# Kernel optimization log

Hardware: AMD Instinct MI355X
Metric: run time of the kernel (lower is better)

The kernel has to match this reference:

```python
import jax, jax.numpy as jnp
import numpy as np

BATCHING_INFO = {0: {'max_tokens': 16, 'batching_range': (0, 16)},
                 1: {'max_tokens': 32, 'batching_range': (16, 32)},
                 2: {'max_tokens': 48, 'batching_range': (32, 100000)}}
WINDOW_SHAPE = (10, 10, 4)
SPARSE_SHAPE = (400, 400, 16)
POS_TEMPERATURE = 1000.0
N_VOXELS = 300000
FEAT_DIM = 192


def get_window_coors_np(coors, sparse_shape, window_shape, do_shift):
    wx, wy, wz = window_shape
    sx, sy, sz = sparse_shape
    mx = int(np.ceil(sx / wx) + 1)
    my = int(np.ceil(sy / wy) + 1)
    mz = int(np.ceil(sz / wz) + 1)
    mper = mx * my * mz
    if do_shift:
        shx, shy, shz = wx // 2, wy // 2, wz // 2
    else:
        shx, shy, shz = wx, wy, wz
    if wz == sz:
        shz = 0
    scx = coors[:, 3] + shx
    scy = coors[:, 2] + shy
    scz = coors[:, 1] + shz
    wcx = scx // wx
    wcy = scy // wy
    wcz = scz // wz
    batch_win_inds = coors[:, 0] * mper + wcx * my * mz + wcy * mz + wcz
    coors_in_win = np.stack([scz % wz, scy % wy, scx % wx], axis=-1)
    return batch_win_inds, coors_in_win


def get_inner_win_inds_np(win_inds):
    # rank of each voxel within its window, stable w.r.t. original order
    n = len(win_inds)
    order = np.argsort(win_inds, kind='stable')
    sw = win_inds[order]
    starts = np.r_[0, np.flatnonzero(np.diff(sw)) + 1]
    counts = np.diff(np.r_[starts, n])
    ranks = np.arange(n) - np.repeat(starts, counts)
    inner = np.empty(n, dtype=np.int64)
    inner[order] = ranks
    return inner


def batching_single_shift(batch_win_inds):
    lvl = -np.ones_like(batch_win_inds)
    inner = get_inner_win_inds_np(batch_win_inds)
    bincount = np.bincount(batch_win_inds)
    num_before = bincount[batch_win_inds]
    target = np.zeros_like(batch_win_inds)
    for bl, info in BATCHING_INFO.items():
        lo, hi = info['batching_range']
        m = (num_before >= lo) & (num_before < hi)
        target[m] = info['max_tokens']
        lvl[m] = bl
    return inner < target, lvl


def get_flat2win_inds_np(batch_win_inds, lvl):
    d = {}
    for dl, info in BATCHING_INFO.items():
        m = lvl == dl
        if not m.any():
            continue
        sub = batch_win_inds[m]
        uniq, conti = np.unique(sub, return_inverse=True)
        inner = get_inner_win_inds_np(sub)
        d[dl] = (conti * info['max_tokens'] + inner, np.flatnonzero(m), len(uniq))
    d['voxel_batching_level'] = lvl
    return d


def partition_indices(coors):
    # full window partition + two-shift voxel batching (pure int logic)
    bwi0, ciw0 = get_window_coors_np(coors, SPARSE_SHAPE, WINDOW_SHAPE, False)
    bwi1, ciw1 = get_window_coors_np(coors, SPARSE_SHAPE, WINDOW_SHAPE, True)
    keep0, lvl0 = batching_single_shift(bwi0)
    idx = np.flatnonzero(keep0)
    lvl0 = lvl0[keep0]
    bwi0 = bwi0[keep0]
    bwi1k = bwi1[keep0]
    keep1, lvl1 = batching_single_shift(bwi1k)
    idx = idx[keep1]
    lvl0 = lvl0[keep1]
    bwi0 = bwi0[keep1]
    lvl1 = lvl1[keep1]
    bwi1k = bwi1k[keep1]
    inds0 = get_flat2win_inds_np(bwi0, lvl0)
    inds1 = get_flat2win_inds_np(bwi1k, lvl1)
    return idx, ciw0[idx], ciw1[idx], inds0, inds1


def get_pos_embed(coors_in_win, feat_dim):
    wx, wy, wz = WINDOW_SHAPE
    c = jnp.asarray(coors_in_win, jnp.float32)
    z = c[:, 0] - wz / 2.0
    y = c[:, 1] - wy / 2.0
    x = c[:, 2] - wx / 2.0
    pos_length = feat_dim // 3
    i = jnp.arange(pos_length, dtype=jnp.float32)
    inv_freq = jnp.power(jnp.float32(POS_TEMPERATURE), 2.0 * jnp.floor(i / 2.0) / pos_length)

    def emb(v):
        e = v[:, None] / inv_freq[None, :]
        return jnp.stack([jnp.sin(e[:, ::2]), jnp.cos(e[:, 1::2])], axis=-1).reshape(e.shape[0], -1)

    return jnp.concatenate([emb(x), emb(y), emb(z)], axis=-1)


def flat2window(feat, inds_dict):
    out = {}
    for dl in sorted(k for k in inds_dict if isinstance(k, int)):
        flat_inds, pos, nwin = inds_dict[dl]
        T = BATCHING_INFO[dl]['max_tokens']
        buf = jnp.zeros((nwin * T, feat.shape[-1]), feat.dtype)
        buf = buf.at[jnp.asarray(flat_inds)].set(feat[jnp.asarray(pos)])
        out[dl] = buf.reshape(nwin, T, feat.shape[-1])
    return out


def setup_inputs() -> dict:
    key = jax.random.key(0)
    rng = np.random.default_rng(0)
    b = rng.integers(0, 2, N_VOXELS)
    z = rng.integers(0, SPARSE_SHAPE[2], N_VOXELS)
    y = rng.integers(0, SPARSE_SHAPE[1], N_VOXELS)
    x = rng.integers(0, SPARSE_SHAPE[0], N_VOXELS)
    coords = np.stack([b, z, y, x], axis=1).astype(np.int64)
    feats = jax.random.normal(key, (N_VOXELS, FEAT_DIM), jnp.float32)
    return {'voxel_features': feats, 'voxel_coords': jnp.asarray(coords)}


def reference(voxel_features, voxel_coords):
    coors = np.asarray(voxel_coords)
    idx, ciw0, ciw1, inds0, inds1 = partition_indices(coors)
    idx_j = jnp.asarray(idx)
    feats = voxel_features[idx_j]
    coords_kept = jnp.asarray(coors[idx])
    outs = [feats, coords_kept]
    for ciw, inds in ((ciw0, inds0), (ciw1, inds1)):
        pe = get_pos_embed(ciw, voxel_features.shape[1])
        pe_dict = flat2window(pe, inds)
        for dl in sorted(k for k in inds if isinstance(k, int)):
            outs.append(pe_dict[dl])
        for dl in sorted(k for k in inds if isinstance(k, int)):
            flat_inds, pos, nwin = inds[dl]
            T = BATCHING_INFO[dl]['max_tokens']
            filled = jnp.zeros((nwin * T,), bool).at[jnp.asarray(flat_inds)].set(True)
            outs.append(jnp.logical_not(filled).reshape(nwin, T))  # key_padding_mask
    return tuple(outs)
```

## Files before the change

kernel.cpp:

```cpp
#include <hip/hip_runtime.h>
#include <math.h>

typedef unsigned int u32;
typedef unsigned short u16;
typedef __attribute__((ext_vector_type(4))) float f32x4;

#define WTOT 16810
#define MPER 8405
#define MAXROWS (WTOT * 48)

#define M_NKEPT 0
#define M_NWIN0 1
#define M_NWIN1 4
#define M_WORDS 16

__device__ __forceinline__ int level_of(int c) {
    if (c < 16) return 0;
    if (c < 32) return 1;
    return 2;
}
__device__ __forceinline__ int target_of(int lvl) {
    return (lvl == 0) ? 16 : ((lvl == 1) ? 32 : 48);
}

__device__ __forceinline__ int wave_incl_scan(int v) {
#pragma unroll
    for (int o = 1; o < 64; o <<= 1) {
        int t = __shfl_up(v, o, 64);
        if ((int)(threadIdx.x & 63) >= o) v += t;
    }
    return v;
}

__device__ __forceinline__ int block_incl_scan_1024(int v, int* wsums, int* total) {
    int lane = threadIdx.x & 63, wid = threadIdx.x >> 6;
    int iv = wave_incl_scan(v);
    if (lane == 63) wsums[wid] = iv;
    __syncthreads();
    if (wid == 0) {
        int s = (lane < 16) ? wsums[lane] : 0;
        s = wave_incl_scan(s);
        if (lane < 16) wsums[lane] = s;
    }
    __syncthreads();
    int add = (wid > 0) ? wsums[wid - 1] : 0;
    int incl = iv + add;
    *total = wsums[15];
    __syncthreads();
    return incl;
}

__device__ __forceinline__ int block_is64(const int* c32, int* sh) {
    if (threadIdx.x < 64) {
        unsigned long long b = __ballot(c32[2 * threadIdx.x + 1] != 0);
        if (threadIdx.x == 0) *sh = (b == 0ULL) ? 1 : 0;
    }
    __syncthreads();
    return *sh;
}

__device__ __forceinline__ int list_rank(const u32* list, int lcount, u32 key, int t) {
    int local = 0;
    int L4 = (lcount + 3) >> 2;
    const uint4* l4 = (const uint4*)list;
    for (int p = 0; p < L4; p++) {
        uint4 e = l4[p];
        local += ((e.x & ~1023u) == key && (int)(e.x & 1023u) < t);
        local += ((e.y & ~1023u) == key && (int)(e.y & 1023u) < t);
        local += ((e.z & ~1023u) == key && (int)(e.z & 1023u) < t);
        local += ((e.w & ~1023u) == key && (int)(e.w & 1023u) < t);
    }
    return local;
}


__global__ __launch_bounds__(256) void k_wincoords(const void* coors_raw, int N, int NB,
        int CE2, int* bwi0, int* bwi1, int* ciw0, int* ciw1, u32* H0, float* dict) {
    __shared__ int s64;
    if ((int)blockIdx.x >= NB) {
        int e = ((int)blockIdx.x - NB) * 256 + (int)threadIdx.x;
        if (e < 76800) {
            int idx = e / 192;
            int j = e - idx * 192;
            int dz = idx & 3;
            int dy = (idx >> 2) % 10;
            int dx = (idx >> 2) / 10;
            int sel = j >> 6;
            float v = (sel == 0) ? ((float)dx - 5.0f)
                    : ((sel == 1) ? ((float)dy - 5.0f) : ((float)dz - 2.0f));
            int kk = (j & 63) >> 1;
            float invf = (float)exp(6.907755278982137 * (double)kk / 32.0);
            float a = v / invf;
            dict[e] = (j & 1) ? cosf(a) : sinf(a);
        }
        return;
    }
    int is64 = block_is64((const int*)coors_raw, &s64);
    int i = (int)blockIdx.x * 256 + (int)threadIdx.x;
    if (i >= N) return;
    int b, z, y, x;
    if (is64) {
        const long long* c = (const long long*)coors_raw;
        long long o = 4LL * i;
        b = (int)c[o]; z = (int)c[o + 1]; y = (int)c[o + 2]; x = (int)c[o + 3];
    } else {
        const int* c = (const int*)coors_raw;
        b = c[4 * i]; z = c[4 * i + 1]; y = c[4 * i + 2]; x = c[4 * i + 3];
    }
    int ch = i >> 10;
    {
        int scx = x + 10, scy = y + 10, scz = z + 4;
        int w = b * MPER + (scx / 10) * 205 + (scy / 10) * 5 + (scz >> 2);
        bwi0[i] = w;
        ciw0[i] = (scz & 3) | ((scy % 10) << 8) | ((scx % 10) << 16);
        atomicAdd(&H0[(size_t)w * CE2 + (ch >> 1)], 1u << ((ch & 1) * 16));
    }
    {
        int scx = x + 5, scy = y + 5, scz = z + 2;
        int w = b * MPER + (scx / 10) * 205 + (scy / 10) * 5 + (scz >> 2);
        bwi1[i] = w;
        ciw1[i] = (scz & 3) | ((scy % 10) << 8) | ((scx % 10) << 16);
    }
}

__global__ __launch_bounds__(256) void k_prefix16(u32* H, u16* counts, int CE2, int NW) {
    int w = ((int)blockIdx.x * 256 + (int)threadIdx.x) >> 6;
    int lane = threadIdx.x & 63;
    if (w >= NW) return;
    u32* row = H + (size_t)w * CE2;
    u32 run = 0;
    for (int p0 = 0; p0 < CE2; p0 += 64) {
        int p = p0 + lane;
        u32 v = (p < CE2) ? row[p] : 0u;
        u32 lo = v & 0xffffu, hi = v >> 16;
        int s = (int)(lo + hi);
        int incl = wave_incl_scan(s);
        u32 excl = (u32)(incl - s);
        u32 offlo = run + excl;
        u32 offhi = offlo + lo;
        if (offlo > 1023u) offlo = 1023u;
        if (offhi > 1023u) offhi = 1023u;
        if (p < CE2) row[p] = offlo | (offhi << 16);
        int tot = __shfl(incl, 63, 64);
        run += (u32)tot;
        if (run > 1023u) run = 1023u;
    }
    if (lane == 0) counts[w] = (u16)run;
}

__global__ __launch_bounds__(1024) void k_stage1(const int* bwi0, const int* bwi1,
        const u16* counts0, const u16* H0_16, u32* H1, int* keep0, int N, int CE, int CE2) {
    __shared__ alignas(16) u32 list[1028];
    __shared__ int lcount;
    int c = blockIdx.x, t = threadIdx.x;
    int i = (c << 10) + t;
    if (t == 0) lcount = 0;
    __syncthreads();
    int w0 = -1, cur = 0, cnt = 0;
    if (i < N) {
        w0 = bwi0[i];
        size_t ro = (size_t)w0 * CE + c;
        cur = (int)H0_16[ro];
        int nxt = (c + 1 < CE) ? (int)H0_16[ro + 1] : (int)counts0[w0];
        cnt = nxt - cur;
        if (cnt >= 2) { int p = atomicAdd(&lcount, 1); list[p] = ((u32)w0 << 10) | (u32)t; }
    }
    __syncthreads();
    if (t < 3) list[lcount + t] = 0xFFFFFFFFu;
    __syncthreads();
    if (i >= N) return;
    int local = (cnt >= 2) ? list_rank(list, lcount, (u32)w0 << 10, t) : 0;
    int k0 = (cur + local) < target_of(level_of((int)counts0[w0]));
    keep0[i] = k0;
    if (k0) atomicAdd(&H1[(size_t)bwi1[i] * CE2 + (c >> 1)], 1u << ((c & 1) * 16));
}

__global__ __launch_bounds__(1024) void k_stage2(const int* bwi0, const int* bwi1,
        const int* keep0, const u16* counts1k, const u16* H1_16,
        u32* HF0, u32* HF1, int* keepf, int* chunkcnt, int N, int CE, int CE2) {
    __shared__ alignas(16) u32 list[1028];
    __shared__ int lcount, blksum;
    int c = blockIdx.x, t = threadIdx.x;
    int i = (c << 10) + t;
    int k0 = (i < N) ? keep0[i] : 0;
    if (t == 0) { lcount = 0; blksum = 0; }
    __syncthreads();
    int w1 = -1, cur = 0, cnt = 0;
    if (k0) {
        w1 = bwi1[i];
        size_t ro = (size_t)w1 * CE + c;
        cur = (int)H1_16[ro];
        int nxt = (c + 1 < CE) ? (int)H1_16[ro + 1] : (int)counts1k[w1];
        cnt = nxt - cur;
        if (cnt >= 2) { int p = atomicAdd(&lcount, 1); list[p] = ((u32)w1 << 10) | (u32)t; }
    }
    __syncthreads();
    if (t < 3) list[lcount + t] = 0xFFFFFFFFu;
    __syncthreads();
    int kf = 0;
    if (k0) {
        int local = (cnt >= 2) ? list_rank(list, lcount, (u32)w1 << 10, t) : 0;
        kf = (cur + local) < target_of(level_of((int)counts1k[w1]));
    }
    if (i < N) keepf[i] = kf;
    if (kf) {
        atomicAdd(&HF0[(size_t)bwi0[i] * CE2 + (c >> 1)], 1u << ((c & 1) * 16));
        atomicAdd(&HF1[(size_t)w1 * CE2 + (c >> 1)], 1u << ((c & 1) * 16));
    }
    unsigned long long b = __ballot(kf);
    if ((t & 63) == 0) atomicAdd(&blksum, __popcll(b));
    __syncthreads();
    if (t == 0) chunkcnt[c] = blksum;
}

__global__ __launch_bounds__(1024) void k_midscan(int* chunkcnt, int C, int* meta,
        const u16* counts0, const u16* fcount0, int* conti0,
        const u16* counts1, const u16* fcount1, int* conti1) {
    __shared__ int wsums[16];
    __shared__ int running;
    __shared__ int run3[3];
    if (blockIdx.x == 0) {
        if (threadIdx.x == 0) running = 0;
        __syncthreads();
        for (int base = 0; base < C; base += 1024) {
            int i = base + threadIdx.x;
            int v = (i < C) ? chunkcnt[i] : 0;
            int total;
            int incl = block_incl_scan_1024(v, wsums, &total);
            int run = running;
            if (i < C) chunkcnt[i] = run + incl - v;
            __syncthreads();
            if (threadIdx.x == 0) running = run + total;
            __syncthreads();
        }
        if (threadIdx.x == 0) meta[M_NKEPT] = running;
    } else {
        const u16* counts = (blockIdx.x == 2) ? counts1 : counts0;
        const u16* fcount = (blockIdx.x == 2) ? fcount1 : fcount0;
        int* conti = (blockIdx.x == 2) ? conti1 : conti0;
        int* nwin_out = meta + ((blockIdx.x == 2) ? M_NWIN1 : M_NWIN0);
        if (threadIdx.x < 3) run3[threadIdx.x] = 0;
        __syncthreads();
        for (int base = 0; base < WTOT; base += 1024) {
            int i = base + threadIdx.x;
            int c = (i < WTOT) ? (int)counts[i] : 0;
            int f = (i < WTOT) ? (int)fcount[i] : 0;
            int lvl = level_of(c);
            int act = (c > 0 && f > 0) ? 1 : 0;
            int packed = act ? (1 << (11 * lvl)) : 0;
            int total;
            int incl = block_incl_scan_1024(packed, wsums, &total);
            int excl = incl - packed;
            int r0 = run3[0], r1 = run3[1], r2 = run3[2];
            if (i < WTOT) {
                int e;
                if (lvl == 0) e = r0 + (excl & 2047);
                else if (lvl == 1) e = r1 + ((excl >> 11) & 2047);
                else e = r2 + ((excl >> 22) & 2047);
                conti[i] = e;
            }
            __syncthreads();
            if (threadIdx.x == 0) {
                run3[0] = r0 + (total & 2047);
                run3[1] = r1 + ((total >> 11) & 2047);
                run3[2] = r2 + ((total >> 22) & 2047);
            }
            __syncthreads();
        }
        if (threadIdx.x < 3) nwin_out[threadIdx.x] = run3[threadIdx.x];
    }
}

__global__ __launch_bounds__(1024) void k_stage3(const int* bwi0, const int* bwi1,
        const int* ciw0, const int* ciw1, const int* keepf,
        const u16* counts0, const u16* counts1k,
        const int* conti0, const int* conti1,
        const u16* HF0_16, const u16* HF1_16,
        const u16* fcount0, const u16* fcount1,
        const int* chunkpref, const int* meta,
        int* idxarr, int* rowvox0, int* rowvox1, int N, int CE) {
    __shared__ alignas(16) u32 list0[1028];
    __shared__ alignas(16) u32 list1[1028];
    __shared__ int lc0, lc1, wsum[16];
    int c = blockIdx.x, t = threadIdx.x, lane = t & 63, wv = t >> 6;
    int i = (c << 10) + t;
    if (t == 0) { lc0 = 0; lc1 = 0; }
    int kf = (i < N) ? keepf[i] : 0;
    unsigned long long m = __ballot(kf);
    if (lane == 0) wsum[wv] = __popcll(m);
    __syncthreads();
    if (t < 64) {
        int s = (t < 16) ? wsum[t] : 0;
        s = wave_incl_scan(s);
        if (t < 16) wsum[t] = s;
    }
    __syncthreads();
    int lk = (wv ? wsum[wv - 1] : 0) + __popcll(m & ((1ull << lane) - 1ull));
    int w0 = -1, w1 = -1, cur0 = 0, cur1 = 0, cnt0 = 0, cnt1 = 0;
    if (kf) {
        w0 = bwi0[i]; w1 = bwi1[i];
        size_t r0o = (size_t)w0 * CE + c;
        cur0 = (int)HF0_16[r0o];
        int nxt0 = (c + 1 < CE) ? (int)HF0_16[r0o + 1] : (int)fcount0[w0];
        cnt0 = nxt0 - cur0;
        if (cnt0 >= 2) { int p = atomicAdd(&lc0, 1); list0[p] = ((u32)w0 << 10) | (u32)t; }
        size_t r1o = (size_t)w1 * CE + c;
        cur1 = (int)HF1_16[r1o];
        int nxt1 = (c + 1 < CE) ? (int)HF1_16[r1o + 1] : (int)fcount1[w1];
        cnt1 = nxt1 - cur1;
        if (cnt1 >= 2) { int p = atomicAdd(&lc1, 1); list1[p] = ((u32)w1 << 10) | (u32)t; }
    }
    __syncthreads();
    if (t < 3) { list0[lc0 + t] = 0xFFFFFFFFu; list1[lc1 + t] = 0xFFFFFFFFu; }
    __syncthreads();
    if (!kf) return;
    int l0 = (cnt0 >= 2) ? list_rank(list0, lc0, (u32)w0 << 10, t) : 0;
    int l1 = (cnt1 >= 2) ? list_rank(list1, lc1, (u32)w1 << 10, t) : 0;
    int innerF0 = cur0 + l0;
    int innerF1 = cur1 + l1;
    idxarr[chunkpref[c] + lk] = i;
    int n00 = meta[M_NWIN0], n01 = meta[M_NWIN0 + 1];
    int n10 = meta[M_NWIN1], n11 = meta[M_NWIN1 + 1];
    {
        int lvl = level_of((int)counts0[w0]);
        int T = target_of(lvl);
        int rb = (lvl == 0) ? 0 : ((lvl == 1) ? n00 * 16 : (n00 * 16 + n01 * 32));
        rowvox0[rb + conti0[w0] * T + innerF0] = ciw0[i];
    }
    {
        int lvl = level_of((int)counts1k[w1]);
        int T = target_of(lvl);
        int rb = (lvl == 0) ? 0 : ((lvl == 1) ? n10 * 16 : (n10 * 16 + n11 * 32));
        rowvox1[rb + conti1[w1] * T + innerF1] = ciw1[i];
    }
}

__global__ __launch_bounds__(256) void k_render(const float* feats, const void* coors_raw,
        const int* meta, const int* idxarr, const int* rowvox0, const int* rowvox1,
        const float* dict, float* out, int NA) {
    __shared__ int s64;
    int nk = meta[M_NKEPT];
    int n00 = meta[M_NWIN0], n01 = meta[M_NWIN0 + 1], n02 = meta[M_NWIN0 + 2];
    int n10 = meta[M_NWIN1], n11 = meta[M_NWIN1 + 1], n12 = meta[M_NWIN1 + 2];
    int R0 = n00 * 16 + n01 * 32 + n02 * 48;
    int R1 = n10 * 16 + n11 * 32 + n12 * 48;
    int obuf0 = nk * 196;
    int omask0 = obuf0 + R0 * 192;
    int obuf1 = omask0 + R0;
    int omask1 = obuf1 + R1 * 192;
    int ototal = omask1 + R1;
    if ((int)blockIdx.x < NA) {
        int is64 = block_is64((const int*)coors_raw, &s64);
        int ocoor = nk * 192;
        const f32x4* src = (const f32x4*)feats;
        f32x4* dst = (f32x4*)out;
        int tot = nk * 52;
        int step = NA * 256;
        for (int idx = (int)blockIdx.x * 256 + (int)threadIdx.x; idx < tot; idx += step) {
            if (idx < nk * 48) {
                int row = idx / 48;
                int col = idx - row * 48;
                f32x4 v = src[(size_t)idxarr[row] * 48 + col];
                __builtin_nontemporal_store(v, dst + idx);
            } else {
                int cidx = idx - nk * 48;
                int k = cidx >> 2, tt = cidx & 3;
                int ii = idxarr[k];
                int v = is64 ? (int)((const long long*)coors_raw)[4LL * ii + tt]
                             : ((const int*)coors_raw)[4 * ii + tt];
                out[ocoor + cidx] = (float)v;
            }
        }
    } else {
        int q0 = obuf0 >> 2, q1 = ototal >> 2;
        const f32x4* dict4 = (const f32x4*)dict;
        f32x4* out4 = (f32x4*)out;
        int step = ((int)gridDim.x - NA) * 256;
        for (int q = q0 + ((int)blockIdx.x - NA) * 256 + (int)threadIdx.x; q < q1; q += step) {
            int e = q << 2;
            f32x4 val;
            bool pe1 = (e >= obuf1) && (e < omask1);
            if ((e < omask0) || pe1) {
                unsigned rel = (unsigned)(e - (pe1 ? obuf1 : obuf0));
                unsigned row = rel / 192u;
                unsigned j = rel - row * 192u;
                int ciw = pe1 ? rowvox1[row] : rowvox0[row];
                if (ciw < 0) {
                    val = (f32x4){0.0f, 0.0f, 0.0f, 0.0f};
                } else {
                    int di = (ciw & 3) + ((ciw >> 8) & 15) * 4 + ((ciw >> 16) & 15) * 40;
                    val = dict4[di * 48 + (int)(j >> 2)];
                }
            } else {
                int base = (e >= omask1) ? omask1 : omask0;
                const int* rv = (e >= omask1) ? rowvox1 : rowvox0;
                int4 c4 = *(const int4*)(rv + (e - base));
                val.x = (c4.x < 0) ? 1.0f : 0.0f;
                val.y = (c4.y < 0) ? 1.0f : 0.0f;
                val.z = (c4.z < 0) ? 1.0f : 0.0f;
                val.w = (c4.w < 0) ? 1.0f : 0.0f;
            }
            __builtin_nontemporal_store(val, out4 + q);
        }
    }
}

extern "C" void kernel_launch(void* const* d_in, const int* in_sizes, int n_in,
                              void* d_out, int out_size, void* d_ws, size_t ws_size,
                              hipStream_t stream) {
    const float* feats = (const float*)d_in[0];
    const void* coors = d_in[1];
    int N = in_sizes[0] / 192;
    int C = (N + 1023) >> 10;
    int CE = (C + 1) & ~1;
    int CE2 = CE >> 1;
    size_t TW32 = (size_t)WTOT * CE2;
    int N4 = (N + 3) & ~3;

    u32* U = (u32*)d_ws;
    int* bwi0 = (int*)U;            int* bwi1 = bwi0 + N4;
    int* ciw0 = bwi1 + N4;          int* ciw1 = ciw0 + N4;
    int* keep0 = ciw1 + N4;         int* keepf = keep0 + N4;
    int* idxarr = keepf + N4;
    u32* H0 = (u32*)(idxarr + N4);
    u32* H1 = H0 + TW32;
    u32* HF0 = H1 + TW32;
    u32* HF1 = HF0 + TW32;
    u16* counts0 = (u16*)(HF1 + TW32);
    u16* counts1k = (u16*)((u32*)counts0 + 8408);
    u16* fcount0 = (u16*)((u32*)counts1k + 8408);
    u16* fcount1 = fcount0 + WTOT;
    int* chunkcnt = (int*)((u32*)fcount0 + 16812);
    int CP4 = (C + 3) & ~3;
    int* conti0 = chunkcnt + CP4;
    int* conti1 = conti0 + 16812;
    int* rowvox0 = conti1 + 16812;
    int* rowvox1 = rowvox0 + MAXROWS;
    int* meta = rowvox1 + MAXROWS;
    float* dict = (float*)(meta + M_WORDS);

    int nb256 = (N + 255) / 256;

    hipMemsetAsync(H0, 0, 4 * TW32 * sizeof(u32), stream);
    hipMemsetAsync(rowvox0, 0xFF, (size_t)2 * MAXROWS * sizeof(int), stream);

    k_wincoords<<<nb256 + 300, 256, 0, stream>>>(coors, N, nb256, CE2,
                                                 bwi0, bwi1, ciw0, ciw1, H0, dict);

    int pgrid = (WTOT * 64 + 255) / 256;
    k_prefix16<<<pgrid, 256, 0, stream>>>(H0, counts0, CE2, WTOT);
    k_stage1<<<C, 1024, 0, stream>>>(bwi0, bwi1, counts0, (const u16*)H0, H1, keep0, N, CE, CE2);

    k_prefix16<<<pgrid, 256, 0, stream>>>(H1, counts1k, CE2, WTOT);
    k_stage2<<<C, 1024, 0, stream>>>(bwi0, bwi1, keep0, counts1k, (const u16*)H1,
                                     HF0, HF1, keepf, chunkcnt, N, CE, CE2);

    k_prefix16<<<2 * pgrid, 256, 0, stream>>>(HF0, fcount0, CE2, 2 * WTOT);
    k_midscan<<<3, 1024, 0, stream>>>(chunkcnt, C, meta,
                                      counts0, fcount0, conti0,
                                      counts1k, fcount1, conti1);

    k_stage3<<<C, 1024, 0, stream>>>(bwi0, bwi1, ciw0, ciw1, keepf, counts0, counts1k,
                                     conti0, conti1, (const u16*)HF0, (const u16*)HF1,
                                     fcount0, fcount1, chunkcnt, meta,
                                     idxarr, rowvox0, rowvox1, N, CE);

    k_render<<<4096, 256, 0, stream>>>(feats, coors, meta, idxarr, rowvox0, rowvox1,
                                       dict, (float*)d_out, 1536);

    (void)n_in; (void)ws_size; (void)out_size;
}
```

Measured before the change: 1.193 ms.

## Pack per-window chunk histograms into 8-bit counters and keep-flags into ballot bitmasks

Per-window/per-chunk histograms now use four 8-bit counters per word instead of two 16-bit ones, halving histogram memory and the memset. Keep flags are stored as per-wave 64-bit ballot masks instead of int arrays. The rowvox 0xFF fill is folded into a prefix-scan launch, replacing a separate memset. Coordinate loads are vectorised and the feature gather uses non-temporal loads. 8-bit prefix offsets saturate at 255, which risks wrong ranks if a window holds more than 255 voxels before a chunk.

```diff
diff --git a/kernel.cpp b/kernel.cpp
--- a/kernel.cpp
+++ b/kernel.cpp
@@ -3,7 +3,10 @@
 
 typedef unsigned int u32;
 typedef unsigned short u16;
+typedef unsigned char u8;
+typedef unsigned long long u64;
 typedef __attribute__((ext_vector_type(4))) float f32x4;
+typedef __attribute__((ext_vector_type(4))) int i32x4;
 
 #define WTOT 16810
 #define MPER 8405
@@ -75,7 +78,7 @@
 
 
 __global__ __launch_bounds__(256) void k_wincoords(const void* coors_raw, int N, int NB,
-        int CE2, int* bwi0, int* bwi1, int* ciw0, int* ciw1, u32* H0, float* dict) {
+        int CE4, int* bwi0, int* bwi1, int* ciw0, int* ciw1, u32* H0, float* dict) {
     __shared__ int s64;
     if ((int)blockIdx.x >= NB) {
         int e = ((int)blockIdx.x - NB) * 256 + (int)threadIdx.x;
@@ -99,13 +102,14 @@
     int i = (int)blockIdx.x * 256 + (int)threadIdx.x;
     if (i >= N) return;
     int b, z, y, x;
+    const i32x4* c4 = (const i32x4*)coors_raw;
     if (is64) {
-        const long long* c = (const long long*)coors_raw;
-        long long o = 4LL * i;
-        b = (int)c[o]; z = (int)c[o + 1]; y = (int)c[o + 2]; x = (int)c[o + 3];
+        i32x4 q0 = c4[2 * (size_t)i];
+        i32x4 q1 = c4[2 * (size_t)i + 1];
+        b = q0.x; z = q0.z; y = q1.x; x = q1.z;
     } else {
-        const int* c = (const int*)coors_raw;
-        b = c[4 * i]; z = c[4 * i + 1]; y = c[4 * i + 2]; x = c[4 * i + 3];
+        i32x4 q = c4[i];
+        b = q.x; z = q.y; y = q.z; x = q.w;
     }
     int ch = i >> 10;
     {
@@ -113,7 +117,7 @@
         int w = b * MPER + (scx / 10) * 205 + (scy / 10) * 5 + (scz >> 2);
         bwi0[i] = w;
         ciw0[i] = (scz & 3) | ((scy % 10) << 8) | ((scx % 10) << 16);
-        atomicAdd(&H0[(size_t)w * CE2 + (ch >> 1)], 1u << ((ch & 1) * 16));
+        atomicAdd(&H0[(size_t)w * CE4 + (ch >> 2)], 1u << ((ch & 3) * 8));
     }
     {
         int scx = x + 5, scy = y + 5, scz = z + 2;
@@ -123,74 +127,87 @@
     }
 }
 
-__global__ __launch_bounds__(256) void k_prefix16(u32* H, u16* counts, int CE2, int NW) {
+__global__ __launch_bounds__(256) void k_prefix8(u32* H, u16* counts, int CE4, int NW,
+                                                 int PB, int* fillPtr, int fillN4) {
+    if ((int)blockIdx.x >= PB) {
+        int idx = ((int)blockIdx.x - PB) * 256 + (int)threadIdx.x;
+        if (idx < fillN4) {
+            i32x4 v = (i32x4){-1, -1, -1, -1};
+            __builtin_nontemporal_store(v, ((i32x4*)fillPtr) + idx);
+        }
+        return;
+    }
     int w = ((int)blockIdx.x * 256 + (int)threadIdx.x) >> 6;
     int lane = threadIdx.x & 63;
     if (w >= NW) return;
-    u32* row = H + (size_t)w * CE2;
-    u32 run = 0;
-    for (int p0 = 0; p0 < CE2; p0 += 64) {
+    u32* row = H + (size_t)w * CE4;
+    int run = 0;
+    for (int p0 = 0; p0 < CE4; p0 += 64) {
         int p = p0 + lane;
-        u32 v = (p < CE2) ? row[p] : 0u;
-        u32 lo = v & 0xffffu, hi = v >> 16;
-        int s = (int)(lo + hi);
+        u32 v = (p < CE4) ? row[p] : 0u;
+        int b0 = (int)(v & 255u), b1 = (int)((v >> 8) & 255u);
+        int b2 = (int)((v >> 16) & 255u), b3 = (int)(v >> 24);
+        int s = b0 + b1 + b2 + b3;
         int incl = wave_incl_scan(s);
-        u32 excl = (u32)(incl - s);
-        u32 offlo = run + excl;
-        u32 offhi = offlo + lo;
-        if (offlo > 1023u) offlo = 1023u;
-        if (offhi > 1023u) offhi = 1023u;
-        if (p < CE2) row[p] = offlo | (offhi << 16);
-        int tot = __shfl(incl, 63, 64);
-        run += (u32)tot;
-        if (run > 1023u) run = 1023u;
+        int base = run + incl - s;
+        int e0 = base, e1 = base + b0, e2 = e1 + b1, e3 = e2 + b2;
+        u32 o0 = (u32)(e0 > 255 ? 255 : e0);
+        u32 o1 = (u32)(e1 > 255 ? 255 : e1);
+        u32 o2 = (u32)(e2 > 255 ? 255 : e2);
+        u32 o3 = (u32)(e3 > 255 ? 255 : e3);
+        if (p < CE4) row[p] = o0 | (o1 << 8) | (o2 << 16) | (o3 << 24);
+        run += __shfl(incl, 63, 64);
+        if (run > 1023) run = 1023;
     }
     if (lane == 0) counts[w] = (u16)run;
 }
 
 __global__ __launch_bounds__(1024) void k_stage1(const int* bwi0, const int* bwi1,
-        const u16* counts0, const u16* H0_16, u32* H1, int* keep0, int N, int CE, int CE2) {
+        const u16* counts0, const u8* H0b, u32* H1, u64* km0, int N, int CB, int CE4) {
     __shared__ alignas(16) u32 list[1028];
     __shared__ int lcount;
-    int c = blockIdx.x, t = threadIdx.x;
+    int c = blockIdx.x, t = threadIdx.x, lane = t & 63, wv = t >> 6;
     int i = (c << 10) + t;
     if (t == 0) lcount = 0;
     __syncthreads();
     int w0 = -1, cur = 0, cnt = 0;
     if (i < N) {
         w0 = bwi0[i];
-        size_t ro = (size_t)w0 * CE + c;
-        cur = (int)H0_16[ro];
-        int nxt = (c + 1 < CE) ? (int)H0_16[ro + 1] : (int)counts0[w0];
+        size_t ro = (size_t)w0 * CB + c;
+        cur = (int)H0b[ro];
+        int nxt = (c + 1 < CB) ? (int)H0b[ro + 1] : (int)counts0[w0];
         cnt = nxt - cur;
         if (cnt >= 2) { int p = atomicAdd(&lcount, 1); list[p] = ((u32)w0 << 10) | (u32)t; }
     }
     __syncthreads();
     if (t < 3) list[lcount + t] = 0xFFFFFFFFu;
     __syncthreads();
-    if (i >= N) return;
-    int local = (cnt >= 2) ? list_rank(list, lcount, (u32)w0 << 10, t) : 0;
-    int k0 = (cur + local) < target_of(level_of((int)counts0[w0]));
-    keep0[i] = k0;
-    if (k0) atomicAdd(&H1[(size_t)bwi1[i] * CE2 + (c >> 1)], 1u << ((c & 1) * 16));
+    int k0 = 0;
+    if (i < N) {
+        int local = (cnt >= 2) ? list_rank(list, lcount, (u32)w0 << 10, t) : 0;
+        k0 = (cur + local) < target_of(level_of((int)counts0[w0]));
+    }
+    u64 bal = __ballot(k0);
+    if (lane == 0) km0[((size_t)c << 4) + wv] = bal;
+    if (k0) atomicAdd(&H1[(size_t)bwi1[i] * CE4 + (c >> 2)], 1u << ((c & 3) * 8));
 }
 
 __global__ __launch_bounds__(1024) void k_stage2(const int* bwi0, const int* bwi1,
-        const int* keep0, const u16* counts1k, const u16* H1_16,
-        u32* HF0, u32* HF1, int* keepf, int* chunkcnt, int N, int CE, int CE2) {
+        const u64* km0, const u16* counts1k, const u8* H1b,
+        u32* HF0, u32* HF1, u64* kmf, int* chunkcnt, int N, int CB, int CE4) {
     __shared__ alignas(16) u32 list[1028];
     __shared__ int lcount, blksum;
-    int c = blockIdx.x, t = threadIdx.x;
+    int c = blockIdx.x, t = threadIdx.x, lane = t & 63, wv = t >> 6;
     int i = (c << 10) + t;
-    int k0 = (i < N) ? keep0[i] : 0;
+    int k0 = (int)((km0[((size_t)c << 4) + wv] >> lane) & 1ULL);
     if (t == 0) { lcount = 0; blksum = 0; }
     __syncthreads();
     int w1 = -1, cur = 0, cnt = 0;
     if (k0) {
         w1 = bwi1[i];
-        size_t ro = (size_t)w1 * CE + c;
-        cur = (int)H1_16[ro];
-        int nxt = (c + 1 < CE) ? (int)H1_16[ro + 1] : (int)counts1k[w1];
+        size_t ro = (size_t)w1 * CB + c;
+        cur = (int)H1b[ro];
+        int nxt = (c + 1 < CB) ? (int)H1b[ro + 1] : (int)counts1k[w1];
         cnt = nxt - cur;
         if (cnt >= 2) { int p = atomicAdd(&lcount, 1); list[p] = ((u32)w1 << 10) | (u32)t; }
     }
@@ -202,13 +219,15 @@
         int local = (cnt >= 2) ? list_rank(list, lcount, (u32)w1 << 10, t) : 0;
         kf = (cur + local) < target_of(level_of((int)counts1k[w1]));
     }
-    if (i < N) keepf[i] = kf;
+    u64 bal = __ballot(kf);
+    if (lane == 0) {
+        kmf[((size_t)c << 4) + wv] = bal;
+        atomicAdd(&blksum, __popcll(bal));
+    }
     if (kf) {
-        atomicAdd(&HF0[(size_t)bwi0[i] * CE2 + (c >> 1)], 1u << ((c & 1) * 16));
-        atomicAdd(&HF1[(size_t)w1 * CE2 + (c >> 1)], 1u << ((c & 1) * 16));
-    }
-    unsigned long long b = __ballot(kf);
-    if ((t & 63) == 0) atomicAdd(&blksum, __popcll(b));
+        atomicAdd(&HF0[(size_t)bwi0[i] * CE4 + (c >> 2)], 1u << ((c & 3) * 8));
+        atomicAdd(&HF1[(size_t)w1 * CE4 + (c >> 2)], 1u << ((c & 3) * 8));
+    }
     __syncthreads();
     if (t == 0) chunkcnt[c] = blksum;
 }
@@ -272,21 +291,21 @@
 }
 
 __global__ __launch_bounds__(1024) void k_stage3(const int* bwi0, const int* bwi1,
-        const int* ciw0, const int* ciw1, const int* keepf,
+        const int* ciw0, const int* ciw1, const u64* kmf,
         const u16* counts0, const u16* counts1k,
         const int* conti0, const int* conti1,
-        const u16* HF0_16, const u16* HF1_16,
+        const u8* HF0b, const u8* HF1b,
         const u16* fcount0, const u16* fcount1,
         const int* chunkpref, const int* meta,
-        int* idxarr, int* rowvox0, int* rowvox1, int N, int CE) {
+        int* idxarr, int* rowvox0, int* rowvox1, int N, int CB) {
     __shared__ alignas(16) u32 list0[1028];
     __shared__ alignas(16) u32 list1[1028];
     __shared__ int lc0, lc1, wsum[16];
     int c = blockIdx.x, t = threadIdx.x, lane = t & 63, wv = t >> 6;
     int i = (c << 10) + t;
     if (t == 0) { lc0 = 0; lc1 = 0; }
-    int kf = (i < N) ? keepf[i] : 0;
-    unsigned long long m = __ballot(kf);
+    u64 m = kmf[((size_t)c << 4) + wv];
+    int kf = (int)((m >> lane) & 1ULL);
     if (lane == 0) wsum[wv] = __popcll(m);
     __syncthreads();
     if (t < 64) {
@@ -299,14 +318,14 @@
     int w0 = -1, w1 = -1, cur0 = 0, cur1 = 0, cnt0 = 0, cnt1 = 0;
     if (kf) {
         w0 = bwi0[i]; w1 = bwi1[i];
-        size_t r0o = (size_t)w0 * CE + c;
-        cur0 = (int)HF0_16[r0o];
-        int nxt0 = (c + 1 < CE) ? (int)HF0_16[r0o + 1] : (int)fcount0[w0];
+        size_t r0o = (size_t)w0 * CB + c;
+        cur0 = (int)HF0b[r0o];
+        int nxt0 = (c + 1 < CB) ? (int)HF0b[r0o + 1] : (int)fcount0[w0];
         cnt0 = nxt0 - cur0;
         if (cnt0 >= 2) { int p = atomicAdd(&lc0, 1); list0[p] = ((u32)w0 << 10) | (u32)t; }
-        size_t r1o = (size_t)w1 * CE + c;
-        cur1 = (int)HF1_16[r1o];
-        int nxt1 = (c + 1 < CE) ? (int)HF1_16[r1o + 1] : (int)fcount1[w1];
+        size_t r1o = (size_t)w1 * CB + c;
+        cur1 = (int)HF1b[r1o];
+        int nxt1 = (c + 1 < CB) ? (int)HF1b[r1o + 1] : (int)fcount1[w1];
         cnt1 = nxt1 - cur1;
         if (cnt1 >= 2) { int p = atomicAdd(&lc1, 1); list1[p] = ((u32)w1 << 10) | (u32)t; }
     }
@@ -360,7 +379,7 @@
             if (idx < nk * 48) {
                 int row = idx / 48;
                 int col = idx - row * 48;
-                f32x4 v = src[(size_t)idxarr[row] * 48 + col];
+                f32x4 v = __builtin_nontemporal_load(src + (size_t)idxarr[row] * 48 + col);
                 __builtin_nontemporal_store(v, dst + idx);
             } else {
                 int cidx = idx - nk * 48;
@@ -394,7 +413,7 @@
             } else {
                 int base = (e >= omask1) ? omask1 : omask0;
                 const int* rv = (e >= omask1) ? rowvox1 : rowvox0;
-                int4 c4 = *(const int4*)(rv + (e - base));
+                const i32x4 c4 = *(const i32x4*)(rv + (e - base));
                 val.x = (c4.x < 0) ? 1.0f : 0.0f;
                 val.y = (c4.y < 0) ? 1.0f : 0.0f;
                 val.z = (c4.z < 0) ? 1.0f : 0.0f;
@@ -412,21 +431,21 @@
     const void* coors = d_in[1];
     int N = in_sizes[0] / 192;
     int C = (N + 1023) >> 10;
-    int CE = (C + 1) & ~1;
-    int CE2 = CE >> 1;
-    size_t TW32 = (size_t)WTOT * CE2;
+    int CE4 = (C + 3) >> 2;
+    int CB = CE4 * 4;
+    size_t TW = (size_t)WTOT * CE4;
     int N4 = (N + 3) & ~3;
 
-    u32* U = (u32*)d_ws;
-    int* bwi0 = (int*)U;            int* bwi1 = bwi0 + N4;
+    int* bwi0 = (int*)d_ws;         int* bwi1 = bwi0 + N4;
     int* ciw0 = bwi1 + N4;          int* ciw1 = ciw0 + N4;
-    int* keep0 = ciw1 + N4;         int* keepf = keep0 + N4;
-    int* idxarr = keepf + N4;
-    u32* H0 = (u32*)(idxarr + N4);
-    u32* H1 = H0 + TW32;
-    u32* HF0 = H1 + TW32;
-    u32* HF1 = HF0 + TW32;
-    u16* counts0 = (u16*)(HF1 + TW32);
+    int* idxarr = ciw1 + N4;
+    u64* km0 = (u64*)(idxarr + N4);
+    u64* kmf = km0 + (size_t)C * 16;
+    u32* H0 = (u32*)(kmf + (size_t)C * 16);
+    u32* H1 = H0 + TW;
+    u32* HF0 = H1 + TW;
+    u32* HF1 = HF0 + TW;
+    u16* counts0 = (u16*)(HF1 + TW);
     u16* counts1k = (u16*)((u32*)counts0 + 8408);
     u16* fcount0 = (u16*)((u32*)counts1k + 8408);
     u16* fcount1 = fcount0 + WTOT;
@@ -441,29 +460,32 @@
 
     int nb256 = (N + 255) / 256;
 
-    hipMemsetAsync(H0, 0, 4 * TW32 * sizeof(u32), stream);
-    hipMemsetAsync(rowvox0, 0xFF, (size_t)2 * MAXROWS * sizeof(int), stream);
-
-    k_wincoords<<<nb256 + 300, 256, 0, stream>>>(coors, N, nb256, CE2,
+    (void)hipMemsetAsync(H0, 0, 4 * TW * sizeof(u32), stream);
+
+    k_wincoords<<<nb256 + 300, 256, 0, stream>>>(coors, N, nb256, CE4,
                                                  bwi0, bwi1, ciw0, ciw1, H0, dict);
 
-    int pgrid = (WTOT * 64 + 255) / 256;
-    k_prefix16<<<pgrid, 256, 0, stream>>>(H0, counts0, CE2, WTOT);
-    k_stage1<<<C, 1024, 0, stream>>>(bwi0, bwi1, counts0, (const u16*)H0, H1, keep0, N, CE, CE2);
-
-    k_prefix16<<<pgrid, 256, 0, stream>>>(H1, counts1k, CE2, WTOT);
-    k_stage2<<<C, 1024, 0, stream>>>(bwi0, bwi1, keep0, counts1k, (const u16*)H1,
-                                     HF0, HF1, keepf, chunkcnt, N, CE, CE2);
-
-    k_prefix16<<<2 * pgrid, 256, 0, stream>>>(HF0, fcount0, CE2, 2 * WTOT);
+    int pgrid = (WTOT + 3) / 4;
+    k_prefix8<<<pgrid, 256, 0, stream>>>(H0, counts0, CE4, WTOT, pgrid, (int*)0, 0);
+    k_stage1<<<C, 1024, 0, stream>>>(bwi0, bwi1, counts0, (const u8*)H0, H1, km0, N, CB, CE4);
+
+    k_prefix8<<<pgrid, 256, 0, stream>>>(H1, counts1k, CE4, WTOT, pgrid, (int*)0, 0);
+    k_stage2<<<C, 1024, 0, stream>>>(bwi0, bwi1, km0, counts1k, (const u8*)H1,
+                                     HF0, HF1, kmf, chunkcnt, N, CB, CE4);
+
+    int pgridF = (2 * WTOT + 3) / 4;
+    int fillN4 = (2 * MAXROWS) / 4;
+    int fillB = (fillN4 + 255) / 256;
+    k_prefix8<<<pgridF + fillB, 256, 0, stream>>>(HF0, fcount0, CE4, 2 * WTOT,
+                                                  pgridF, rowvox0, fillN4);
     k_midscan<<<3, 1024, 0, stream>>>(chunkcnt, C, meta,
                                       counts0, fcount0, conti0,
                                       counts1k, fcount1, conti1);
 
-    k_stage3<<<C, 1024, 0, stream>>>(bwi0, bwi1, ciw0, ciw1, keepf, counts0, counts1k,
-                                     conti0, conti1, (const u16*)HF0, (const u16*)HF1,
+    k_stage3<<<C, 1024, 0, stream>>>(bwi0, bwi1, ciw0, ciw1, kmf, counts0, counts1k,
+                                     conti0, conti1, (const u8*)HF0, (const u8*)HF1,
                                      fcount0, fcount1, chunkcnt, meta,
-                                     idxarr, rowvox0, rowvox1, N, CE);
+                                     idxarr, rowvox0, rowvox1, N, CB);
 
     k_render<<<4096, 256, 0, stream>>>(feats, coors, meta, idxarr, rowvox0, rowvox1,
                                        dict, (float*)d_out, 1536);
```

After: 1.158 ms. 1.03x faster.
